# Performance work log

Measured on AMD Instinct MI355X. Metric: run time of the kernel, lower is better.

Reference implementation:

```python
import jax, jax.numpy as jnp
import numpy as np

C = 1.0            # curvature args.c
EPS = 1e-7         # Hyperboloid eps for float32
MIN_NORM = 1e-15
MAX_SQDIST = 50.0
NUM_LAYERS = 3     # args.num_layers (resSumGCN hops)
MARGIN = 0.1       # args.margin
N_NODES = 200000
NUM_USERS = 100000
EMB_DIM = 64
E_ADJ = 1600000
E_TR = 65536
NUM_NEG = 16


def _mink_dot(x, y, keepdim=True):
    # Minkowski inner product: -x0*y0 + sum_i xi*yi
    res = jnp.sum(x * y, axis=-1) - 2.0 * x[..., 0] * y[..., 0]
    return res[..., None] if keepdim else res


def _sqdist(x, y, c):
    K = 1.0 / c
    prod = _mink_dot(x, y)                      # [E, 1]
    theta = jnp.maximum(-prod / K, 1.0 + EPS)
    return jnp.minimum(K * jnp.arccosh(theta) ** 2, MAX_SQDIST)


def _expmap0(u, c):
    sqrtK = (1.0 / c) ** 0.5
    x = u[..., 1:]
    x_norm = jnp.maximum(jnp.linalg.norm(x, axis=-1, keepdims=True), MIN_NORM)
    theta = x_norm / sqrtK
    first = sqrtK * jnp.cosh(theta)
    rest = sqrtK * jnp.sinh(theta) * x / x_norm
    return jnp.concatenate([first, rest], axis=-1)


def _logmap0(x, c):
    sqrtK = (1.0 / c) ** 0.5
    y = x[..., 1:]
    y_norm = jnp.maximum(jnp.linalg.norm(y, axis=-1, keepdims=True), MIN_NORM)
    theta = jnp.maximum(x[..., :1] / sqrtK, 1.0 + EPS)
    rest = sqrtK * jnp.arccosh(theta) * y / y_norm
    return jnp.concatenate([jnp.zeros_like(rest[..., :1]), rest], axis=-1)


def _proj(x, c):
    K = 1.0 / c
    y = x[..., 1:]
    first = jnp.sqrt(K + jnp.sum(y * y, axis=-1, keepdims=True))
    return jnp.concatenate([first, y], axis=-1)


def setup_inputs() -> dict:
    key = jax.random.key(0)
    ks = jax.random.split(key, 8)
    # embedding init: uniform(-scale, scale) tangent vector, then expmap0 onto hyperboloid
    tan = jax.random.uniform(ks[0], (N_NODES, EMB_DIM), minval=-0.1, maxval=0.1, dtype=jnp.float32)
    weight = _expmap0(tan, C)
    adj_row = jnp.sort(jax.random.randint(ks[1], (E_ADJ,), 0, N_NODES, dtype=jnp.int32))
    adj_col = jax.random.randint(ks[2], (E_ADJ,), 0, N_NODES, dtype=jnp.int32)
    # mimic symmetric-normalized adjacency values (~1/deg)
    adj_vals = jax.random.uniform(ks[3], (E_ADJ,), dtype=jnp.float32) * 0.125
    anchor = jax.random.randint(ks[4], (E_TR,), 0, NUM_USERS, dtype=jnp.int32)
    pos = jax.random.randint(ks[5], (E_TR,), 0, NUM_USERS, dtype=jnp.int32) + NUM_USERS
    neg = jax.random.randint(ks[6], (E_TR, NUM_NEG), 0, NUM_USERS, dtype=jnp.int32) + NUM_USERS
    return {"weight": weight, "adj_vals": adj_vals, "adj_row": adj_row,
            "adj_col": adj_col, "anchor": anchor, "pos": pos, "neg": neg}


def _encode(weight, adj_row, adj_col, adj_vals):
    # HypAgg: logmap0 -> resSumGCN (sum of adj^k x for k=1..L) -> expmap0 -> proj
    x_t = _logmap0(weight, C)
    h = x_t
    acc = jnp.zeros_like(x_t)
    for _ in range(NUM_LAYERS):
        h = jax.ops.segment_sum(adj_vals[:, None] * h[adj_col], adj_row,
                                num_segments=N_NODES, indices_are_sorted=True)
        acc = acc + h
    return _proj(_expmap0(acc, C), C)


def reference(weight, adj_vals, adj_row, adj_col, anchor, pos, neg):
    h = _encode(weight, adj_row, adj_col, adj_vals)      # [N, d] on hyperboloid
    emb_a = h[anchor]                                    # [E, d]
    emb_p = h[pos]                                       # [E, d]
    # decode_pos: sqdist + hratio weight
    pos_scores = _sqdist(emb_a, emb_p, C)                # [E, 1]
    u0 = emb_a[:, 0]
    i0 = emb_p[:, 0]
    score = (1.0 - _mink_dot(emb_a, emb_p, keepdim=False) - u0 - i0) / (u0 * i0)
    w = jax.nn.sigmoid(-score)[:, None]                  # [E, 1]
    # decode_neg: hard-negative mining (euclidean sqdist to positive, take min)
    d2 = jnp.sum((h[neg] - emb_p[:, None, :]) ** 2, axis=-1)   # [E, num_neg]
    hard_idx = jnp.argmin(d2, axis=1)
    hard_neg = jnp.take_along_axis(neg, hard_idx[:, None], axis=1)[:, 0]
    neg_scores = _sqdist(emb_a, h[hard_neg], C)          # [E, 1]
    # margin ranking loss with hyperbolic-ratio weight
    loss = jnp.sum(jnp.maximum(pos_scores - neg_scores + MARGIN * w, 0.0))
    return loss
```

## Files before the change

kernel.cpp:

```cpp
#include <hip/hip_runtime.h>
#include <hip/hip_bf16.h>
#include <math.h>

#define N_NODES 200000
#define EMB_DIM 64
#define E_ADJ 1600000
#define E_TR 65536
#define NUM_NEG 16
#define EPS 1e-7f
#define MIN_NORM 1e-15f
#define MAX_SQDIST 50.0f
#define MARGIN 0.1f
#define EPW 8
#define LOSS_BLOCKS (E_TR / (4 * EPW))
#define NPART (E_TR / 4)
#define SPMM_BLOCKS 2048
#define NWAVES (SPMM_BLOCKS * 4)
#define RPW 25
#define LDS_CAP 512

#define PACK_BLOCKS ((E_ADJ + 255) / 256)
#define RP_BLOCKS   ((N_NODES + 1 + 255) / 256)
#define LOG_BLOCKS  ((N_NODES + 15) / 16)

typedef float f4 __attribute__((ext_vector_type(4)));

__device__ __forceinline__ float group_reduce16(float v) {
    v += __shfl_xor(v, 8, 64);
    v += __shfl_xor(v, 4, 64);
    v += __shfl_xor(v, 2, 64);
    v += __shfl_xor(v, 1, 64);
    return v;
}

__device__ __forceinline__ float group_reduce8(float v) {
    v += __shfl_xor(v, 4, 64);
    v += __shfl_xor(v, 2, 64);
    v += __shfl_xor(v, 1, 64);
    return v;
}

__device__ __forceinline__ float dot4(f4 a, f4 b) {
    return a.x * b.x + a.y * b.y + a.z * b.z + a.w * b.w;
}

__device__ __forceinline__ unsigned bfr(float f) {
    unsigned u = __float_as_uint(f);
    return (u + 0x7fffu + ((u >> 16) & 1u)) >> 16;
}
__device__ __forceinline__ uint2 f42bf(f4 v) {
    return make_uint2(bfr(v.x) | (bfr(v.y) << 16), bfr(v.z) | (bfr(v.w) << 16));
}
__device__ __forceinline__ f4 bf2f4(uint2 g) {
    f4 r;
    r.x = __uint_as_float(g.x << 16);
    r.y = __uint_as_float(g.x & 0xffff0000u);
    r.z = __uint_as_float(g.y << 16);
    r.w = __uint_as_float(g.y & 0xffff0000u);
    return r;
}

__device__ __forceinline__ void fma8(f4& a0, f4& a1, uint4 g, float v) {
    f4 lo, hi;
    lo.x = __uint_as_float(g.x << 16);
    lo.y = __uint_as_float(g.x & 0xffff0000u);
    lo.z = __uint_as_float(g.y << 16);
    lo.w = __uint_as_float(g.y & 0xffff0000u);
    hi.x = __uint_as_float(g.z << 16);
    hi.y = __uint_as_float(g.z & 0xffff0000u);
    hi.z = __uint_as_float(g.w << 16);
    hi.w = __uint_as_float(g.w & 0xffff0000u);
    a0 += lo * v;
    a1 += hi * v;
}

__global__ void prelude_kernel(const int* __restrict__ cols, const float* __restrict__ vals,
                               int2* __restrict__ ev, const int* __restrict__ rows,
                               int* __restrict__ rp, const float* __restrict__ w,
                               uint2* __restrict__ xt) {
    int b = blockIdx.x;
    if (b < PACK_BLOCKS) {
        int i = b * 256 + threadIdx.x;
        if (i < E_ADJ) ev[i] = make_int2(cols[i] << 3, __float_as_int(vals[i]));
    } else if (b < PACK_BLOCKS + RP_BLOCKS) {
        int r = (b - PACK_BLOCKS) * 256 + threadIdx.x;
        if (r <= N_NODES) {
            int lo = 0, hi = E_ADJ;
            while (lo < hi) {
                int mid = (lo + hi) >> 1;
                if (rows[mid] < r) lo = mid + 1; else hi = mid;
            }
            rp[r] = lo;
        }
    } else {
        int bb = b - PACK_BLOCKS - RP_BLOCKS;
        int wave = bb * 4 + (threadIdx.x >> 6);
        int lane = threadIdx.x & 63;
        int e = lane >> 4, d = lane & 15;
        int node = wave * 4 + e;
        if (node < N_NODES) {
            f4 v = ((const f4*)w)[(node << 4) + d];
            f4 y = v;
            if (d == 0) y.x = 0.0f;
            float n2 = group_reduce16(dot4(y, y));
            float ynorm = fmaxf(sqrtf(n2), MIN_NORM);
            float w0 = __shfl(v.x, lane & 48, 64);
            float theta = fmaxf(w0, 1.0f + EPS);
            float scale = acoshf(theta) / ynorm;
            xt[(node << 4) + d] = f42bf(y * scale);
        }
    }
}

__device__ __forceinline__ void row_accum_lds(f4& a0, f4& a1,
                                              const uint4* __restrict__ h_in,
                                              const int2* L, int s, int e, int d) {
    int k = s;
    for (; k + 2 <= e; k += 2) {
        int2 cv0 = L[k];
        int2 cv1 = L[k + 1];
        uint4 g0 = h_in[cv0.x + d];
        uint4 g1 = h_in[cv1.x + d];
        fma8(a0, a1, g0, __int_as_float(cv0.y));
        fma8(a0, a1, g1, __int_as_float(cv1.y));
    }
    if (k < e) {
        int2 cv = L[k];
        fma8(a0, a1, h_in[cv.x + d], __int_as_float(cv.y));
    }
}

__device__ __forceinline__ void row_accum_glb(f4& a0, f4& a1,
                                              const uint4* __restrict__ h_in,
                                              const int2* __restrict__ ev,
                                              int s, int e, int d) {
    int k = s;
    for (; k + 2 <= e; k += 2) {
        int2 cv0 = ev[k];
        int2 cv1 = ev[k + 1];
        uint4 g0 = h_in[cv0.x + d];
        uint4 g1 = h_in[cv1.x + d];
        fma8(a0, a1, g0, __int_as_float(cv0.y));
        fma8(a0, a1, g1, __int_as_float(cv1.y));
    }
    if (k < e) {
        int2 cv = ev[k];
        fma8(a0, a1, h_in[cv.x + d], __int_as_float(cv.y));
    }
}

__global__ __launch_bounds__(256) void spmm_kernel(const uint4* __restrict__ h_in,
                                                   uint4* __restrict__ h_out,
                                                   const int2* __restrict__ ev,
                                                   const int* __restrict__ rp) {
    __shared__ int2 evs[4][LDS_CAP];
    int wib = threadIdx.x >> 6;
    int lane = threadIdx.x & 63;
    int g = lane >> 3, d = lane & 7;
    int wid = __builtin_amdgcn_readfirstlane(blockIdx.x * 4 + wib);
    int r0 = wid * RPW;
    if (r0 >= N_NODES) return;
    int r1 = min(r0 + RPW, N_NODES);
    int ebase = rp[r0];
    int etot  = rp[r1];
    int nst   = etot - ebase;
    bool allst = nst <= LDS_CAP;
    int staged = min(nst, LDS_CAP);
    int2* L = evs[wib];
    for (int k = lane; k < staged; k += 64)
        L[k] = ev[ebase + k];
    __syncthreads();

    for (int base = r0; base < r1; base += 8) {
        int row = base + g;
        bool valid = row < r1;
        int s = 0, e = 0;
        if (valid) { s = rp[row]; e = rp[row + 1]; }
        f4 a0 = {0.f, 0.f, 0.f, 0.f}, a1 = {0.f, 0.f, 0.f, 0.f};
        if (allst) row_accum_lds(a0, a1, h_in, L, s - ebase, e - ebase, d);
        else       row_accum_glb(a0, a1, h_in, ev, s, e, d);
        if (valid) {
            uint2 p0 = f42bf(a0), p1 = f42bf(a1);
            h_out[(row << 3) + d] = make_uint4(p0.x, p0.y, p1.x, p1.y);
        }
    }
}

__global__ __launch_bounds__(256) void spmm_expmap_kernel(const uint4* __restrict__ h_gather,
                                                          const uint4* __restrict__ h1,
                                                          const uint4* __restrict__ h2,
                                                          float* __restrict__ h,
                                                          float* __restrict__ nrm2,
                                                          const int2* __restrict__ ev,
                                                          const int* __restrict__ rp) {
    __shared__ int2 evs[4][LDS_CAP];
    int wib = threadIdx.x >> 6;
    int lane = threadIdx.x & 63;
    int g = lane >> 3, d = lane & 7;
    int wid = __builtin_amdgcn_readfirstlane(blockIdx.x * 4 + wib);
    int r0 = wid * RPW;
    if (r0 >= N_NODES) return;
    int r1 = min(r0 + RPW, N_NODES);
    int ebase = rp[r0];
    int etot  = rp[r1];
    int nst   = etot - ebase;
    bool allst = nst <= LDS_CAP;
    int staged = min(nst, LDS_CAP);
    int2* L = evs[wib];
    for (int k = lane; k < staged; k += 64)
        L[k] = ev[ebase + k];
    __syncthreads();

    for (int base = r0; base < r1; base += 8) {
        int row = base + g;
        bool valid = row < r1;
        int s = 0, e = 0;
        uint4 b1 = make_uint4(0, 0, 0, 0), b2 = make_uint4(0, 0, 0, 0);
        if (valid) {
            s = rp[row]; e = rp[row + 1];
            b1 = h1[(row << 3) + d];
            b2 = h2[(row << 3) + d];
        }
        f4 a0 = {0.f, 0.f, 0.f, 0.f}, a1 = {0.f, 0.f, 0.f, 0.f};
        if (allst) row_accum_lds(a0, a1, h_gather, L, s - ebase, e - ebase, d);
        else       row_accum_glb(a0, a1, h_gather, ev, s, e, d);
        if (valid) {
            f4 h1lo = bf2f4(make_uint2(b1.x, b1.y)), h1hi = bf2f4(make_uint2(b1.z, b1.w));
            f4 h2lo = bf2f4(make_uint2(b2.x, b2.y)), h2hi = bf2f4(make_uint2(b2.z, b2.w));
            f4 u0 = (h1lo + h2lo) + a0;
            f4 u1 = (h1hi + h2hi) + a1;
            f4 x0 = u0, x1 = u1;
            if (d == 0) x0.x = 0.0f;
            float n2 = group_reduce8(dot4(x0, x0) + dot4(x1, x1));
            float xn = fmaxf(sqrtf(n2), MIN_NORM);
            float sh = sinhf(xn);
            float sc = sh / xn;
            f4 rv0 = x0 * sc, rv1 = x1 * sc;
            float rr2 = group_reduce8(dot4(rv0, rv0) + dot4(rv1, rv1));
            float first = sqrtf(1.0f + rr2);
            f4 o0 = rv0, o1 = rv1;
            if (d == 0) o0.x = first;
            ((f4*)h)[(row << 4) + 2 * d]     = o0;
            ((f4*)h)[(row << 4) + 2 * d + 1] = o1;
            if (d == 0) nrm2[row] = first * first + rr2;
        }
    }
}

__global__ __launch_bounds__(256) void loss_kernel(const float* __restrict__ h, const float* __restrict__ nrm2,
                            const int* __restrict__ anchor, const int* __restrict__ pos,
                            const int* __restrict__ neg, float* __restrict__ partials) {
    int wib = threadIdx.x >> 6;
    int lane = threadIdx.x & 63;
    int e = lane >> 4, d = lane & 15;
    int w = __builtin_amdgcn_readfirstlane(blockIdx.x * 4 + wib);
    const f4* H = (const f4*)h;
    int i0 = w * EPW;

    float fdap = 0.0f, fdan = 0.0f, fa0 = 1.0f, fp0 = 1.0f, fn0 = 1.0f;

    #pragma unroll 2
    for (int t = 0; t < EPW; ++t) {
        int i = i0 + t;
        int ia = anchor[i], ip = pos[i];
        f4 a4 = H[(ia << 4) + d];
        f4 p4 = H[(ip << 4) + d];
        int4 nb4 = ((const int4*)(neg + (size_t)i * NUM_NEG))[e];

        float s[4];
        s[0] = dot4(p4, H[(nb4.x << 4) + d]);
        s[1] = dot4(p4, H[(nb4.y << 4) + d]);
        s[2] = dot4(p4, H[(nb4.z << 4) + d]);
        s[3] = dot4(p4, H[(nb4.w << 4) + d]);
        float dap = dot4(a4, p4);

        {
            bool hi = (d & 8) != 0;
            float send0 = hi ? s[0] : s[2];
            float send1 = hi ? s[1] : s[3];
            float r0 = __shfl_xor(send0, 8, 64);
            float r1 = __shfl_xor(send1, 8, 64);
            float k0 = hi ? s[2] : s[0];
            float k1 = hi ? s[3] : s[1];
            s[0] = k0 + r0;
            s[1] = k1 + r1;
        }
        float sv;
        {
            bool hi = (d & 4) != 0;
            float send = hi ? s[0] : s[1];
            float r = __shfl_xor(send, 4, 64);
            float k = hi ? s[1] : s[0];
            sv = k + r;
        }
        sv += __shfl_xor(sv, 2, 64);
        sv += __shfl_xor(sv, 1, 64);
        int b_lane = ((d >> 3) & 1) * 2 + ((d >> 2) & 1);
        int nidx_lane = (d & 8) ? ((d & 4) ? nb4.w : nb4.z)
                                : ((d & 4) ? nb4.y : nb4.x);
        int j_lane = 4 * e + b_lane;

        float np2 = nrm2[ip];
        float bd = nrm2[nidx_lane] + np2 - 2.0f * sv;
        int bj = j_lane;
        #pragma unroll
        for (int off = 32; off > 0; off >>= 1) {
            float od = __shfl_xor(bd, off, 64);
            int   oj = __shfl_xor(bj, off, 64);
            if (od < bd || (od == bd && oj < bj)) { bd = od; bj = oj; }
        }
        int bn = neg[(size_t)i * NUM_NEG + __builtin_amdgcn_readfirstlane(bj)];
        f4 w4 = H[(bn << 4) + d];
        float dan = group_reduce16(dot4(a4, w4));
        dap = group_reduce16(dap);
        float a0 = __shfl(a4.x, 0, 64);
        float p0 = __shfl(p4.x, 0, 64);
        float n0 = __shfl(w4.x, 0, 64);

        bool sel = (lane == t);
        fdap = sel ? dap : fdap;
        fdan = sel ? dan : fdan;
        fa0  = sel ? a0  : fa0;
        fp0  = sel ? p0  : fp0;
        fn0  = sel ? n0  : fn0;
    }

    float mink = fdap - 2.0f * fa0 * fp0;
    float th = fmaxf(-mink, 1.0f + EPS);
    float ac = acoshf(th);
    float pos_score = fminf(ac * ac, MAX_SQDIST);
    float score = (1.0f - mink - fa0 - fp0) / (fa0 * fp0);
    float wgt = 1.0f / (1.0f + expf(score));
    float minkn = fdan - 2.0f * fa0 * fn0;
    float thn = fmaxf(-minkn, 1.0f + EPS);
    float acn = acoshf(thn);
    float neg_score = fminf(acn * acn, MAX_SQDIST);
    float loss = fmaxf(pos_score - neg_score + MARGIN * wgt, 0.0f);

    float pa = ((__shfl(loss, 0, 64) + __shfl(loss, 1, 64)) + __shfl(loss, 2, 64)) + __shfl(loss, 3, 64);
    float pb = ((__shfl(loss, 4, 64) + __shfl(loss, 5, 64)) + __shfl(loss, 6, 64)) + __shfl(loss, 7, 64);
    if (lane == 0) {
        partials[2 * w]     = pa;
        partials[2 * w + 1] = pb;
    }
}

__global__ void reduce_kernel(const float* __restrict__ partials, float* __restrict__ out) {
    int tid = threadIdx.x;
    float s = 0.0f;
    for (int i = tid; i < NPART; i += 1024)
        s += partials[i];
    #pragma unroll
    for (int off = 32; off > 0; off >>= 1)
        s += __shfl_xor(s, off, 64);
    __shared__ float part[16];
    if ((tid & 63) == 0) part[tid >> 6] = s;
    __syncthreads();
    if (tid == 0) {
        float t = 0.0f;
        #pragma unroll
        for (int k = 0; k < 16; ++k) t += part[k];
        out[0] = t;
    }
}

extern "C" void kernel_launch(void* const* d_in, const int* in_sizes, int n_in,
                              void* d_out, int out_size, void* d_ws, size_t ws_size,
                              hipStream_t stream) {
    const float* weight   = (const float*)d_in[0];
    const float* adj_vals = (const float*)d_in[1];
    const int*   adj_row  = (const int*)d_in[2];
    const int*   adj_col  = (const int*)d_in[3];
    const int*   anchor   = (const int*)d_in[4];
    const int*   pos      = (const int*)d_in[5];
    const int*   neg      = (const int*)d_in[6];
    float* out = (float*)d_out;

    const size_t NODEF32 = (size_t)N_NODES * EMB_DIM * sizeof(float);
    const size_t NODEBF  = (size_t)N_NODES * EMB_DIM * sizeof(unsigned short);
    const size_t MB = 1024 * 1024;
    char* ws = (char*)d_ws;
    float* hfin = (float*)(ws);
    uint2* bf0  = (uint2*)(ws + NODEF32);
    char*  bf1  = (char*) (ws + NODEF32 + NODEBF);
    char*  bf2  = (char*) (ws + NODEF32 + 2 * NODEBF);
    int*   rp   = (int*)  (ws + NODEF32 + 3 * NODEBF);
    float* nrm2 = (float*)(ws + NODEF32 + 3 * NODEBF + 1 * MB);
    int2*  ev   = (int2*) (ws + NODEF32 + 3 * NODEBF + 2 * MB);
    float* partials = (float*)(ws + NODEF32 + 3 * NODEBF + 16 * MB);

    prelude_kernel<<<PACK_BLOCKS + RP_BLOCKS + LOG_BLOCKS, 256, 0, stream>>>(
        adj_col, adj_vals, ev, adj_row, rp, weight, bf0);
    spmm_kernel<<<SPMM_BLOCKS, 256, 0, stream>>>((const uint4*)bf0, (uint4*)bf1, ev, rp);
    spmm_kernel<<<SPMM_BLOCKS, 256, 0, stream>>>((const uint4*)bf1, (uint4*)bf2, ev, rp);
    spmm_expmap_kernel<<<SPMM_BLOCKS, 256, 0, stream>>>((const uint4*)bf2, (const uint4*)bf1,
                                                        (const uint4*)bf2, hfin, nrm2, ev, rp);
    loss_kernel<<<LOSS_BLOCKS, 256, 0, stream>>>(hfin, nrm2, anchor, pos, neg, partials);
    reduce_kernel<<<1, 1024, 0, stream>>>(partials, out);
}
```

Measured before the change: 294.6 us.

## Balance SpMM rows across lane groups by edge count and unroll gathers by four

Each wave's 25 rows are now split among its 8 lane-groups by equal shares of edges, found with a binary search over row pointers staged in LDS, instead of round-robin batches of 8 rows. Row pointers are cached in shared memory, and the inner gather loop is unrolled by four to keep more independent loads in flight. This targets load imbalance and divergence from uneven row degrees, plus gather latency. In exchange it adds binary-search overhead, and since groups now run different numbers of rows, the shuffle reductions in the expmap kernel execute under divergent control flow within the wave.

```diff
diff --git a/kernel.cpp b/kernel.cpp
--- a/kernel.cpp
+++ b/kernel.cpp
@@ -15,7 +15,6 @@
 #define LOSS_BLOCKS (E_TR / (4 * EPW))
 #define NPART (E_TR / 4)
 #define SPMM_BLOCKS 2048
-#define NWAVES (SPMM_BLOCKS * 4)
 #define RPW 25
 #define LDS_CAP 512
 
@@ -112,40 +111,79 @@
     }
 }
 
-__device__ __forceinline__ void row_accum_lds(f4& a0, f4& a1,
-                                              const uint4* __restrict__ h_in,
-                                              const int2* L, int s, int e, int d) {
+__device__ __forceinline__ void accum_lds4(f4& a0, f4& a1,
+                                           const uint4* __restrict__ h_in,
+                                           const int2* L, int s, int e, int d) {
     int k = s;
-    for (; k + 2 <= e; k += 2) {
-        int2 cv0 = L[k];
-        int2 cv1 = L[k + 1];
-        uint4 g0 = h_in[cv0.x + d];
-        uint4 g1 = h_in[cv1.x + d];
-        fma8(a0, a1, g0, __int_as_float(cv0.y));
-        fma8(a0, a1, g1, __int_as_float(cv1.y));
+    for (; k + 4 <= e; k += 4) {
+        int2 c0 = L[k], c1 = L[k + 1], c2 = L[k + 2], c3 = L[k + 3];
+        uint4 g0 = h_in[c0.x + d];
+        uint4 g1 = h_in[c1.x + d];
+        uint4 g2 = h_in[c2.x + d];
+        uint4 g3 = h_in[c3.x + d];
+        fma8(a0, a1, g0, __int_as_float(c0.y));
+        fma8(a0, a1, g1, __int_as_float(c1.y));
+        fma8(a0, a1, g2, __int_as_float(c2.y));
+        fma8(a0, a1, g3, __int_as_float(c3.y));
+    }
+    if (k + 2 <= e) {
+        int2 c0 = L[k], c1 = L[k + 1];
+        uint4 g0 = h_in[c0.x + d];
+        uint4 g1 = h_in[c1.x + d];
+        fma8(a0, a1, g0, __int_as_float(c0.y));
+        fma8(a0, a1, g1, __int_as_float(c1.y));
+        k += 2;
     }
     if (k < e) {
-        int2 cv = L[k];
-        fma8(a0, a1, h_in[cv.x + d], __int_as_float(cv.y));
-    }
-}
-
-__device__ __forceinline__ void row_accum_glb(f4& a0, f4& a1,
-                                              const uint4* __restrict__ h_in,
-                                              const int2* __restrict__ ev,
-                                              int s, int e, int d) {
+        int2 c = L[k];
+        fma8(a0, a1, h_in[c.x + d], __int_as_float(c.y));
+    }
+}
+
+__device__ __forceinline__ void accum_glb4(f4& a0, f4& a1,
+                                           const uint4* __restrict__ h_in,
+                                           const int2* __restrict__ ev,
+                                           int s, int e, int d) {
     int k = s;
-    for (; k + 2 <= e; k += 2) {
-        int2 cv0 = ev[k];
-        int2 cv1 = ev[k + 1];
-        uint4 g0 = h_in[cv0.x + d];
-        uint4 g1 = h_in[cv1.x + d];
-        fma8(a0, a1, g0, __int_as_float(cv0.y));
-        fma8(a0, a1, g1, __int_as_float(cv1.y));
+    for (; k + 4 <= e; k += 4) {
+        int2 c0 = ev[k], c1 = ev[k + 1], c2 = ev[k + 2], c3 = ev[k + 3];
+        uint4 g0 = h_in[c0.x + d];
+        uint4 g1 = h_in[c1.x + d];
+        uint4 g2 = h_in[c2.x + d];
+        uint4 g3 = h_in[c3.x + d];
+        fma8(a0, a1, g0, __int_as_float(c0.y));
+        fma8(a0, a1, g1, __int_as_float(c1.y));
+        fma8(a0, a1, g2, __int_as_float(c2.y));
+        fma8(a0, a1, g3, __int_as_float(c3.y));
+    }
+    if (k + 2 <= e) {
+        int2 c0 = ev[k], c1 = ev[k + 1];
+        uint4 g0 = h_in[c0.x + d];
+        uint4 g1 = h_in[c1.x + d];
+        fma8(a0, a1, g0, __int_as_float(c0.y));
+        fma8(a0, a1, g1, __int_as_float(c1.y));
+        k += 2;
     }
     if (k < e) {
-        int2 cv = ev[k];
-        fma8(a0, a1, h_in[cv.x + d], __int_as_float(cv.y));
+        int2 c = ev[k];
+        fma8(a0, a1, h_in[c.x + d], __int_as_float(c.y));
+    }
+}
+
+__device__ __forceinline__ void group_bounds(const int* RPS, int nrows, int ebase,
+                                             int nst, int g, int& gs, int& ge) {
+    gs = 0; ge = nrows;
+    if (g > 0) {
+        int t = ebase + (g * nst) / 8;
+        int lo = 0, hi = nrows;
+        while (lo < hi) { int m = (lo + hi) >> 1; if (RPS[m] < t) lo = m + 1; else hi = m; }
+        gs = lo;
+    }
+    if (g < 7) {
+        int t = ebase + ((g + 1) * nst) / 8;
+        int lo = 0, hi = nrows;
+        while (lo < hi) { int m = (lo + hi) >> 1; if (RPS[m] < t) lo = m + 1; else hi = m; }
+        ge = lo;
     }
 }
 
@@ -154,15 +192,17 @@
                                                    const int2* __restrict__ ev,
                                                    const int* __restrict__ rp) {
     __shared__ int2 evs[4][LDS_CAP];
+    __shared__ int rps[4][RPW + 1];
     int wib = threadIdx.x >> 6;
     int lane = threadIdx.x & 63;
     int g = lane >> 3, d = lane & 7;
     int wid = __builtin_amdgcn_readfirstlane(blockIdx.x * 4 + wib);
     int r0 = wid * RPW;
     if (r0 >= N_NODES) return;
-    int r1 = min(r0 + RPW, N_NODES);
+    int nrows = min(RPW, N_NODES - r0);
+    if (lane <= nrows) rps[wib][lane] = rp[r0 + lane];
     int ebase = rp[r0];
-    int etot  = rp[r1];
+    int etot  = rp[r0 + nrows];
     int nst   = etot - ebase;
     bool allst = nst <= LDS_CAP;
     int staged = min(nst, LDS_CAP);
@@ -170,19 +210,18 @@
     for (int k = lane; k < staged; k += 64)
         L[k] = ev[ebase + k];
     __syncthreads();
-
-    for (int base = r0; base < r1; base += 8) {
-        int row = base + g;
-        bool valid = row < r1;
-        int s = 0, e = 0;
-        if (valid) { s = rp[row]; e = rp[row + 1]; }
+    const int* RPS = rps[wib];
+
+    int gs, ge;
+    group_bounds(RPS, nrows, ebase, nst, g, gs, ge);
+    for (int rr = gs; rr < ge; ++rr) {
+        int row = r0 + rr;
+        int sA = RPS[rr], eA = RPS[rr + 1];
         f4 a0 = {0.f, 0.f, 0.f, 0.f}, a1 = {0.f, 0.f, 0.f, 0.f};
-        if (allst) row_accum_lds(a0, a1, h_in, L, s - ebase, e - ebase, d);
-        else       row_accum_glb(a0, a1, h_in, ev, s, e, d);
-        if (valid) {
-            uint2 p0 = f42bf(a0), p1 = f42bf(a1);
-            h_out[(row << 3) + d] = make_uint4(p0.x, p0.y, p1.x, p1.y);
-        }
+        if (allst) accum_lds4(a0, a1, h_in, L, sA - ebase, eA - ebase, d);
+        else       accum_glb4(a0, a1, h_in, ev, sA, eA, d);
+        uint2 p0 = f42bf(a0), p1 = f42bf(a1);
+        h_out[(row << 3) + d] = make_uint4(p0.x, p0.y, p1.x, p1.y);
     }
 }
 
@@ -194,15 +233,17 @@
                                                           const int2* __restrict__ ev,
                                                           const int* __restrict__ rp) {
     __shared__ int2 evs[4][LDS_CAP];
+    __shared__ int rps[4][RPW + 1];
     int wib = threadIdx.x >> 6;
     int lane = threadIdx.x & 63;
     int g = lane >> 3, d = lane & 7;
     int wid = __builtin_amdgcn_readfirstlane(blockIdx.x * 4 + wib);
     int r0 = wid * RPW;
     if (r0 >= N_NODES) return;
-    int r1 = min(r0 + RPW, N_NODES);
+    int nrows = min(RPW, N_NODES - r0);
+    if (lane <= nrows) rps[wib][lane] = rp[r0 + lane];
     int ebase = rp[r0];
-    int etot  = rp[r1];
+    int etot  = rp[r0 + nrows];
     int nst   = etot - ebase;
     bool allst = nst <= LDS_CAP;
     int staged = min(nst, LDS_CAP);
@@ -210,40 +251,37 @@
     for (int k = lane; k < staged; k += 64)
         L[k] = ev[ebase + k];
     __syncthreads();
-
-    for (int base = r0; base < r1; base += 8) {
-        int row = base + g;
-        bool valid = row < r1;
-        int s = 0, e = 0;
-        uint4 b1 = make_uint4(0, 0, 0, 0), b2 = make_uint4(0, 0, 0, 0);
-        if (valid) {
-            s = rp[row]; e = rp[row + 1];
-            b1 = h1[(row << 3) + d];
-            b2 = h2[(row << 3) + d];
-        }
+    const int* RPS = rps[wib];
+
+    int gs, ge;
+    group_bounds(RPS, nrows, ebase, nst, g, gs, ge);
+    for (int rr = gs; rr < ge; ++rr) {
+        int row = r0 + rr;
+        int sA = RPS[rr], eA = RPS[rr + 1];
+        uint4 b1 = h1[(row << 3) + d];
+        uint4 b2 = h2[(row << 3) + d];
         f4 a0 = {0.f, 0.f, 0.f, 0.f}, a1 = {0.f, 0.f, 0.f, 0.f};
-        if (allst) row_accum_lds(a0, a1, h_gather, L, s - ebase, e - ebase, d);
-        else       row_accum_glb(a0, a1, h_gather, ev, s, e, d);
-        if (valid) {
-            f4 h1lo = bf2f4(make_uint2(b1.x, b1.y)), h1hi = bf2f4(make_uint2(b1.z, b1.w));
-            f4 h2lo = bf2f4(make_uint2(b2.x, b2.y)), h2hi = bf2f4(make_uint2(b2.z, b2.w));
-            f4 u0 = (h1lo + h2lo) + a0;
-            f4 u1 = (h1hi + h2hi) + a1;
-            f4 x0 = u0, x1 = u1;
-            if (d == 0) x0.x = 0.0f;
-            float n2 = group_reduce8(dot4(x0, x0) + dot4(x1, x1));
-            float xn = fmaxf(sqrtf(n2), MIN_NORM);
-            float sh = sinhf(xn);
-            float sc = sh / xn;
-            f4 rv0 = x0 * sc, rv1 = x1 * sc;
-            float rr2 = group_reduce8(dot4(rv0, rv0) + dot4(rv1, rv1));
-            float first = sqrtf(1.0f + rr2);
-            f4 o0 = rv0, o1 = rv1;
-            if (d == 0) o0.x = first;
-            ((f4*)h)[(row << 4) + 2 * d]     = o0;
-            ((f4*)h)[(row << 4) + 2 * d + 1] = o1;
-            if (d == 0) nrm2[row] = first * first + rr2;
-        }
+        if (allst) accum_lds4(a0, a1, h_gather, L, sA - ebase, eA - ebase, d);
+        else       accum_glb4(a0, a1, h_gather, ev, sA, eA, d);
+
+        f4 h1lo = bf2f4(make_uint2(b1.x, b1.y)), h1hi = bf2f4(make_uint2(b1.z, b1.w));
+        f4 h2lo = bf2f4(make_uint2(b2.x, b2.y)), h2hi = bf2f4(make_uint2(b2.z, b2.w));
+        f4 u0 = (h1lo + h2lo) + a0;
+        f4 u1 = (h1hi + h2hi) + a1;
+        f4 x0 = u0, x1 = u1;
+        if (d == 0) x0.x = 0.0f;
+        float n2 = group_reduce8(dot4(x0, x0) + dot4(x1, x1));
+        float xn = fmaxf(sqrtf(n2), MIN_NORM);
+        float sh = sinhf(xn);
+        float sc = sh / xn;
+        f4 rv0 = x0 * sc, rv1 = x1 * sc;
+        float rr2 = group_reduce8(dot4(rv0, rv0) + dot4(rv1, rv1));
+        float first = sqrtf(1.0f + rr2);
+        f4 o0 = rv0, o1 = rv1;
+        if (d == 0) o0.x = first;
+        ((f4*)h)[(row << 4) + 2 * d]     = o0;
+        ((f4*)h)[(row << 4) + 2 * d + 1] = o1;
+        if (d == 0) nrm2[row] = first * first + rr2;
     }
 }
 
```

Result: no change. 297.9 us (+1.1%).

## Stream edges per wave with one lane per feature in SpMM kernels

Applied to the files above, without the earlier changes.

Replaces the 8-rows-per-wave, 8-lanes-per-row SpMM mapping with a scheme where a whole wave walks its block's edges sequentially, each of the 64 lanes owning one bf16 feature and closing rows as edge boundaries pass. Row pointers are staged in LDS, and edge gathers are double-buffered in chunks of four to keep loads in flight. This removes load imbalance between rows of different degree within a wave and the idle lanes on short rows. In exchange each gather becomes a 2-byte-per-lane access, and rows are processed serially, which may reduce memory-level parallelism.

```diff
diff --git a/kernel.cpp b/kernel.cpp
--- a/kernel.cpp
+++ b/kernel.cpp
@@ -15,7 +15,6 @@
 #define LOSS_BLOCKS (E_TR / (4 * EPW))
 #define NPART (E_TR / 4)
 #define SPMM_BLOCKS 2048
-#define NWAVES (SPMM_BLOCKS * 4)
 #define RPW 25
 #define LDS_CAP 512
 
@@ -33,7 +32,10 @@
     return v;
 }
 
-__device__ __forceinline__ float group_reduce8(float v) {
+__device__ __forceinline__ float reduce64(float v) {
+    v += __shfl_xor(v, 32, 64);
+    v += __shfl_xor(v, 16, 64);
+    v += __shfl_xor(v, 8, 64);
     v += __shfl_xor(v, 4, 64);
     v += __shfl_xor(v, 2, 64);
     v += __shfl_xor(v, 1, 64);
@@ -50,28 +52,6 @@
 }
 __device__ __forceinline__ uint2 f42bf(f4 v) {
     return make_uint2(bfr(v.x) | (bfr(v.y) << 16), bfr(v.z) | (bfr(v.w) << 16));
-}
-__device__ __forceinline__ f4 bf2f4(uint2 g) {
-    f4 r;
-    r.x = __uint_as_float(g.x << 16);
-    r.y = __uint_as_float(g.x & 0xffff0000u);
-    r.z = __uint_as_float(g.y << 16);
-    r.w = __uint_as_float(g.y & 0xffff0000u);
-    return r;
-}
-
-__device__ __forceinline__ void fma8(f4& a0, f4& a1, uint4 g, float v) {
-    f4 lo, hi;
-    lo.x = __uint_as_float(g.x << 16);
-    lo.y = __uint_as_float(g.x & 0xffff0000u);
-    lo.z = __uint_as_float(g.y << 16);
-    lo.w = __uint_as_float(g.y & 0xffff0000u);
-    hi.x = __uint_as_float(g.z << 16);
-    hi.y = __uint_as_float(g.z & 0xffff0000u);
-    hi.z = __uint_as_float(g.w << 16);
-    hi.w = __uint_as_float(g.w & 0xffff0000u);
-    a0 += lo * v;
-    a1 += hi * v;
 }
 
 __global__ void prelude_kernel(const int* __restrict__ cols, const float* __restrict__ vals,
@@ -81,7 +61,7 @@
     int b = blockIdx.x;
     if (b < PACK_BLOCKS) {
         int i = b * 256 + threadIdx.x;
-        if (i < E_ADJ) ev[i] = make_int2(cols[i] << 3, __float_as_int(vals[i]));
+        if (i < E_ADJ) ev[i] = make_int2(cols[i] << 6, __float_as_int(vals[i]));
     } else if (b < PACK_BLOCKS + RP_BLOCKS) {
         int r = (b - PACK_BLOCKS) * 256 + threadIdx.x;
         if (r <= N_NODES) {
@@ -112,139 +92,160 @@
     }
 }
 
-__device__ __forceinline__ void row_accum_lds(f4& a0, f4& a1,
-                                              const uint4* __restrict__ h_in,
-                                              const int2* L, int s, int e, int d) {
-    int k = s;
-    for (; k + 2 <= e; k += 2) {
-        int2 cv0 = L[k];
-        int2 cv1 = L[k + 1];
-        uint4 g0 = h_in[cv0.x + d];
-        uint4 g1 = h_in[cv1.x + d];
-        fma8(a0, a1, g0, __int_as_float(cv0.y));
-        fma8(a0, a1, g1, __int_as_float(cv1.y));
-    }
-    if (k < e) {
-        int2 cv = L[k];
-        fma8(a0, a1, h_in[cv.x + d], __int_as_float(cv.y));
-    }
-}
-
-__device__ __forceinline__ void row_accum_glb(f4& a0, f4& a1,
-                                              const uint4* __restrict__ h_in,
-                                              const int2* __restrict__ ev,
-                                              int s, int e, int d) {
-    int k = s;
-    for (; k + 2 <= e; k += 2) {
-        int2 cv0 = ev[k];
-        int2 cv1 = ev[k + 1];
-        uint4 g0 = h_in[cv0.x + d];
-        uint4 g1 = h_in[cv1.x + d];
-        fma8(a0, a1, g0, __int_as_float(cv0.y));
-        fma8(a0, a1, g1, __int_as_float(cv1.y));
-    }
-    if (k < e) {
-        int2 cv = ev[k];
-        fma8(a0, a1, h_in[cv.x + d], __int_as_float(cv.y));
-    }
-}
-
-__global__ __launch_bounds__(256) void spmm_kernel(const uint4* __restrict__ h_in,
-                                                   uint4* __restrict__ h_out,
+
+template <typename F>
+__device__ __forceinline__ void edge_stream_lds(const int2* L, const unsigned short* __restrict__ hs,
+                                                int lane, int nst, const int* RPS, int ebase,
+                                                int nrows, F close_row) {
+    float acc = 0.0f;
+    int ri = 0;
+    int rend = __builtin_amdgcn_readfirstlane(RPS[1]) - ebase;
+    int2 ca[4]; unsigned ga[4];
+    int2 cb[4]; unsigned gb[4];
+    int NC = (nst + 3) >> 2;
+
+    auto FETCH = [&](int base, int2 (&c)[4], unsigned (&g)[4]) {
+        #pragma unroll
+        for (int j = 0; j < 4; ++j) c[j] = L[base + j];
+        #pragma unroll
+        for (int j = 0; j < 4; ++j) g[j] = (unsigned)hs[(unsigned)c[j].x + lane];
+    };
+    auto PROC = [&](int k0, int2 (&c)[4], unsigned (&g)[4]) {
+        #pragma unroll
+        for (int j = 0; j < 4; ++j) {
+            int k = k0 + j;
+            while (rend == k) {
+                close_row(ri, acc);
+                acc = 0.0f;
+                ++ri;
+                rend = (ri < nrows) ? (__builtin_amdgcn_readfirstlane(RPS[ri + 1]) - ebase)
+                                    : 0x7fffffff;
+            }
+            acc += __uint_as_float(g[j] << 16) * __int_as_float(c[j].y);
+        }
+    };
+
+    if (NC > 0) FETCH(0, ca, ga);
+    int c = 0;
+    while (c < NC) {
+        if (c + 1 < NC) FETCH((c + 1) * 4, cb, gb);
+        PROC(c * 4, ca, ga);
+        ++c;
+        if (c >= NC) break;
+        if (c + 1 < NC) FETCH((c + 1) * 4, ca, ga);
+        PROC(c * 4, cb, gb);
+        ++c;
+    }
+    while (ri < nrows) {
+        close_row(ri, acc);
+        acc = 0.0f;
+        ++ri;
+    }
+}
+
+template <typename F>
+__device__ __forceinline__ void edge_stream_glb(const int2* __restrict__ ev, const unsigned short* __restrict__ hs,
+                                                int lane, int nst, const int* RPS, int ebase,
+                                                int nrows, F close_row) {
+    float acc = 0.0f;
+    int ri = 0;
+    int rend = __builtin_amdgcn_readfirstlane(RPS[1]) - ebase;
+    for (int k = 0; k < nst; ++k) {
+        int2 cv = ev[ebase + k];
+        unsigned gg = (unsigned)hs[(unsigned)cv.x + lane];
+        while (rend == k) {
+            close_row(ri, acc);
+            acc = 0.0f;
+            ++ri;
+            rend = (ri < nrows) ? (__builtin_amdgcn_readfirstlane(RPS[ri + 1]) - ebase)
+                                : 0x7fffffff;
+        }
+        acc += __uint_as_float(gg << 16) * __int_as_float(cv.y);
+    }
+    while (ri < nrows) {
+        close_row(ri, acc);
+        acc = 0.0f;
+        ++ri;
+    }
+}
+
+__global__ __launch_bounds__(256) void spmm_kernel(const unsigned short* __restrict__ h_in,
+                                                   unsigned short* __restrict__ h_out,
                                                    const int2* __restrict__ ev,
                                                    const int* __restrict__ rp) {
-    __shared__ int2 evs[4][LDS_CAP];
+    __shared__ int2 evs[4][LDS_CAP + 4];
+    __shared__ int rps[4][RPW + 1];
     int wib = threadIdx.x >> 6;
     int lane = threadIdx.x & 63;
-    int g = lane >> 3, d = lane & 7;
     int wid = __builtin_amdgcn_readfirstlane(blockIdx.x * 4 + wib);
     int r0 = wid * RPW;
     if (r0 >= N_NODES) return;
-    int r1 = min(r0 + RPW, N_NODES);
-    int ebase = rp[r0];
-    int etot  = rp[r1];
-    int nst   = etot - ebase;
+    int nrows = min(RPW, N_NODES - r0);
+    if (lane <= nrows) rps[wib][lane] = rp[r0 + lane];
+    int ebase = __builtin_amdgcn_readfirstlane(rp[r0]);
+    int nst = __builtin_amdgcn_readfirstlane(rp[r0 + nrows]) - ebase;
     bool allst = nst <= LDS_CAP;
-    int staged = min(nst, LDS_CAP);
     int2* L = evs[wib];
-    for (int k = lane; k < staged; k += 64)
-        L[k] = ev[ebase + k];
+    if (allst) {
+        for (int k = lane; k < nst; k += 64) L[k] = ev[ebase + k];
+        if (lane < 4) L[nst + lane] = make_int2(0, 0);
+    }
     __syncthreads();
-
-    for (int base = r0; base < r1; base += 8) {
-        int row = base + g;
-        bool valid = row < r1;
-        int s = 0, e = 0;
-        if (valid) { s = rp[row]; e = rp[row + 1]; }
-        f4 a0 = {0.f, 0.f, 0.f, 0.f}, a1 = {0.f, 0.f, 0.f, 0.f};
-        if (allst) row_accum_lds(a0, a1, h_in, L, s - ebase, e - ebase, d);
-        else       row_accum_glb(a0, a1, h_in, ev, s, e, d);
-        if (valid) {
-            uint2 p0 = f42bf(a0), p1 = f42bf(a1);
-            h_out[(row << 3) + d] = make_uint4(p0.x, p0.y, p1.x, p1.y);
-        }
-    }
-}
-
-__global__ __launch_bounds__(256) void spmm_expmap_kernel(const uint4* __restrict__ h_gather,
-                                                          const uint4* __restrict__ h1,
-                                                          const uint4* __restrict__ h2,
+    const int* RPS = rps[wib];
+
+    auto close = [&](int ri_, float accv) {
+        h_out[(r0 + ri_) * 64 + lane] = (unsigned short)bfr(accv);
+    };
+    if (allst) edge_stream_lds(L, h_in, lane, nst, RPS, ebase, nrows, close);
+    else       edge_stream_glb(ev, h_in, lane, nst, RPS, ebase, nrows, close);
+}
+
+__global__ __launch_bounds__(256) void spmm_expmap_kernel(const unsigned short* __restrict__ h_gather,
+                                                          const unsigned short* __restrict__ h1,
+                                                          const unsigned short* __restrict__ h2,
                                                           float* __restrict__ h,
                                                           float* __restrict__ nrm2,
                                                           const int2* __restrict__ ev,
                                                           const int* __restrict__ rp) {
-    __shared__ int2 evs[4][LDS_CAP];
+    __shared__ int2 evs[4][LDS_CAP + 4];
+    __shared__ int rps[4][RPW + 1];
     int wib = threadIdx.x >> 6;
     int lane = threadIdx.x & 63;
-    int g = lane >> 3, d = lane & 7;
     int wid = __builtin_amdgcn_readfirstlane(blockIdx.x * 4 + wib);
     int r0 = wid * RPW;
     if (r0 >= N_NODES) return;
-    int r1 = min(r0 + RPW, N_NODES);
-    int ebase = rp[r0];
-    int etot  = rp[r1];
-    int nst   = etot - ebase;
+    int nrows = min(RPW, N_NODES - r0);
+    if (lane <= nrows) rps[wib][lane] = rp[r0 + lane];
+    int ebase = __builtin_amdgcn_readfirstlane(rp[r0]);
+    int nst = __builtin_amdgcn_readfirstlane(rp[r0 + nrows]) - ebase;
     bool allst = nst <= LDS_CAP;
-    int staged = min(nst, LDS_CAP);
     int2* L = evs[wib];
-    for (int k = lane; k < staged; k += 64)
-        L[k] = ev[ebase + k];
+    if (allst) {
+        for (int k = lane; k < nst; k += 64) L[k] = ev[ebase + k];
+        if (lane < 4) L[nst + lane] = make_int2(0, 0);
+    }
     __syncthreads();
-
-    for (int base = r0; base < r1; base += 8) {
-        int row = base + g;
-        bool valid = row < r1;
-        int s = 0, e = 0;
-        uint4 b1 = make_uint4(0, 0, 0, 0), b2 = make_uint4(0, 0, 0, 0);
-        if (valid) {
-            s = rp[row]; e = rp[row + 1];
-            b1 = h1[(row << 3) + d];
-            b2 = h2[(row << 3) + d];
-        }
-        f4 a0 = {0.f, 0.f, 0.f, 0.f}, a1 = {0.f, 0.f, 0.f, 0.f};
-        if (allst) row_accum_lds(a0, a1, h_gather, L, s - ebase, e - ebase, d);
-        else       row_accum_glb(a0, a1, h_gather, ev, s, e, d);
-        if (valid) {
-            f4 h1lo = bf2f4(make_uint2(b1.x, b1.y)), h1hi = bf2f4(make_uint2(b1.z, b1.w));
-            f4 h2lo = bf2f4(make_uint2(b2.x, b2.y)), h2hi = bf2f4(make_uint2(b2.z, b2.w));
-            f4 u0 = (h1lo + h2lo) + a0;
-            f4 u1 = (h1hi + h2hi) + a1;
-            f4 x0 = u0, x1 = u1;
-            if (d == 0) x0.x = 0.0f;
-            float n2 = group_reduce8(dot4(x0, x0) + dot4(x1, x1));
-            float xn = fmaxf(sqrtf(n2), MIN_NORM);
-            float sh = sinhf(xn);
-            float sc = sh / xn;
-            f4 rv0 = x0 * sc, rv1 = x1 * sc;
-            float rr2 = group_reduce8(dot4(rv0, rv0) + dot4(rv1, rv1));
-            float first = sqrtf(1.0f + rr2);
-            f4 o0 = rv0, o1 = rv1;
-            if (d == 0) o0.x = first;
-            ((f4*)h)[(row << 4) + 2 * d]     = o0;
-            ((f4*)h)[(row << 4) + 2 * d + 1] = o1;
-            if (d == 0) nrm2[row] = first * first + rr2;
-        }
-    }
+    const int* RPS = rps[wib];
+
+    auto close = [&](int ri_, float accv) {
+        int row = r0 + ri_;
+        float f1 = __uint_as_float((unsigned)h1[row * 64 + lane] << 16);
+        float f2 = __uint_as_float((unsigned)h2[row * 64 + lane] << 16);
+        float u = (f1 + f2) + accv;
+        float x = (lane == 0) ? 0.0f : u;
+        float n2 = reduce64(x * x);
+        float xn = fmaxf(sqrtf(n2), MIN_NORM);
+        float sh = sinhf(xn);
+        float sc = sh / xn;
+        float rv = x * sc;
+        float rr2 = reduce64(rv * rv);
+        float first = sqrtf(1.0f + rr2);
+        float o = (lane == 0) ? first : rv;
+        h[row * 64 + lane] = o;
+        if (lane == 0) nrm2[row] = first * first + rr2;
+    };
+    if (allst) edge_stream_lds(L, h_gather, lane, nst, RPS, ebase, nrows, close);
+    else       edge_stream_glb(ev, h_gather, lane, nst, RPS, ebase, nrows, close);
 }
 
 __global__ __launch_bounds__(256) void loss_kernel(const float* __restrict__ h, const float* __restrict__ nrm2,
@@ -391,10 +392,12 @@
 
     prelude_kernel<<<PACK_BLOCKS + RP_BLOCKS + LOG_BLOCKS, 256, 0, stream>>>(
         adj_col, adj_vals, ev, adj_row, rp, weight, bf0);
-    spmm_kernel<<<SPMM_BLOCKS, 256, 0, stream>>>((const uint4*)bf0, (uint4*)bf1, ev, rp);
-    spmm_kernel<<<SPMM_BLOCKS, 256, 0, stream>>>((const uint4*)bf1, (uint4*)bf2, ev, rp);
-    spmm_expmap_kernel<<<SPMM_BLOCKS, 256, 0, stream>>>((const uint4*)bf2, (const uint4*)bf1,
-                                                        (const uint4*)bf2, hfin, nrm2, ev, rp);
+    spmm_kernel<<<SPMM_BLOCKS, 256, 0, stream>>>((const unsigned short*)bf0, (unsigned short*)bf1, ev, rp);
+    spmm_kernel<<<SPMM_BLOCKS, 256, 0, stream>>>((const unsigned short*)bf1, (unsigned short*)bf2, ev, rp);
+    spmm_expmap_kernel<<<SPMM_BLOCKS, 256, 0, stream>>>((const unsigned short*)bf2,
+                                                        (const unsigned short*)bf1,
+                                                        (const unsigned short*)bf2,
+                                                        hfin, nrm2, ev, rp);
     loss_kernel<<<LOSS_BLOCKS, 256, 0, stream>>>(hfin, nrm2, anchor, pos, neg, partials);
     reduce_kernel<<<1, 1024, 0, stream>>>(partials, out);
 }
```

Result: slower. 327.0 us (+11.0%).
